# Optimization experiments

Measured on AMD Instinct MI355X. Metric: run time of the kernel, lower is better.

Reference implementation:

```python
import jax, jax.numpy as jnp
import numpy as np


def setup_inputs() -> dict:
    key = jax.random.key(0)
    k1, k2 = jax.random.split(key)
    B, H, S, D = 4, 16, 4096, 128
    tensor = jax.random.normal(k1, (B, H, S, D), dtype=jnp.float32)
    # per-head decay in (0, 1)
    gamma = jax.random.uniform(k2, (H,), dtype=jnp.float32)
    return {"tensor": tensor, "gamma": gamma}


def reference(tensor, gamma):
    """Discounted cumsum (left): y[b,h,t,d] = x[b,h,t,d] + gamma[h] * y[b,h,t-1,d].

    Implemented as a parallel associative scan over the sequence axis using the
    linear-recurrence monoid (a, b) o (a', b') = (a*a', a'*b + b').
    """
    # broadcast per-head gamma to element-wise decay coefficients  (B,H,S,D)
    a = jnp.broadcast_to(gamma[None, :, None, None], tensor.shape)

    def combine(c1, c2):
        a1, b1 = c1
        a2, b2 = c2
        return (a1 * a2, a2 * b1 + b2)

    _, y = jax.lax.associative_scan(combine, (a, tensor), axis=2)
    return y
```

## Files before the change

### kernel.cpp

```cpp
#include <hip/hip_runtime.h>

constexpr int B = 4, H = 16, S = 4096, D = 128;
constexpr int BH = B * H;
constexpr int CHUNKS = 128;
constexpr int L = S / CHUNKS;
constexpr int D4 = D / 4;
constexpr int UNITS = BH * CHUNKS;
constexpr int THREADS = UNITS * D4;
constexpr int NBLK = THREADS / 256;

typedef float f32x4 __attribute__((ext_vector_type(4)));

__device__ __forceinline__ float4 f4fma(float a, float4 x, float4 y) {
    float4 r;
    r.x = fmaf(a, x.x, y.x);
    r.y = fmaf(a, x.y, y.y);
    r.z = fmaf(a, x.z, y.z);
    r.w = fmaf(a, x.w, y.w);
    return r;
}

__device__ __forceinline__ void nt_store4(float4* p, float4 v) {
    union { float4 s; f32x4 v4; } u;
    u.s = v;
    __builtin_nontemporal_store(u.v4, (f32x4*)p);
}

__global__ __launch_bounds__(256) void dc_carry(const float4* __restrict__ x,
                                                const float* __restrict__ gamma,
                                                float4* __restrict__ carries) {
    const int tid  = blockIdx.x * 256 + threadIdx.x;
    const int l    = tid & (D4 - 1);
    const int unit = tid >> 5;
    const int bh   = unit >> 7;
    const float g  = gamma[bh & (H - 1)];

    const float lg = __logf(g);
    float kf = (-2.996f + __logf(1.0f - g)) / lg;
    int K = (int)ceilf(kf);
    K = max(1, min(L, K));

    const float4* pe = x + ((size_t)unit * L + (L - K)) * D4 + l;
    float4 carry = make_float4(0.f, 0.f, 0.f, 0.f);
    #pragma unroll 8
    for (int i = 0; i < K; ++i) {
        carry = f4fma(g, carry, pe[(size_t)i * D4]);
    }
    carries[(size_t)unit * D4 + l] = carry;
}

__global__ __launch_bounds__(256) void dc_scan(const float4* __restrict__ x,
                                               const float* __restrict__ gamma,
                                               const float4* __restrict__ carries,
                                               float4* __restrict__ y) {
    const int tid  = blockIdx.x * 256 + threadIdx.x;
    const int l    = tid & (D4 - 1);
    const int unit = tid >> 5;
    const int c    = unit & (CHUNKS - 1);
    const int bh   = unit >> 7;
    const float g  = gamma[bh & (H - 1)];

    float gL = g;
    #pragma unroll
    for (int k = 0; k < 5; ++k) gL *= gL;

    float wf = (-4.828f + __logf(1.0f - gL)) / __logf(gL);
    int W = min(c, max(1, (int)ceilf(wf)));

    const size_t base = (size_t)unit * (L * D4) + l;
    const float4* p = x + base;
    float4*       q = y + base;

    float4 v0 = p[0 * D4];
    float4 v1 = p[1 * D4];
    float4 v2 = p[2 * D4];
    float4 v3 = p[3 * D4];

    const float4* cp = carries + ((size_t)(bh * CHUNKS) + c - 1) * D4 + l;
    float4 P = make_float4(0.f, 0.f, 0.f, 0.f);
    float mult = 1.f;
    for (int k = 0; k < W; ++k) {
        P = f4fma(mult, cp[-(ptrdiff_t)k * D4], P);
        mult *= gL;
    }

    float4 run = P;
    run = f4fma(g, run, v0); nt_store4(q + 0 * D4, run);
    run = f4fma(g, run, v1); nt_store4(q + 1 * D4, run);
    run = f4fma(g, run, v2); nt_store4(q + 2 * D4, run);
    run = f4fma(g, run, v3); nt_store4(q + 3 * D4, run);
    #pragma unroll 7
    for (int i = 4; i < L; ++i) {
        run = f4fma(g, run, p[(size_t)i * D4]);
        nt_store4(q + (size_t)i * D4, run);
    }
}

extern "C" void kernel_launch(void* const* d_in, const int* in_sizes, int n_in,
                              void* d_out, int out_size, void* d_ws, size_t ws_size,
                              hipStream_t stream) {
    const float4* x     = (const float4*)d_in[0];
    const float*  gamma = (const float*)d_in[1];
    float4*       y     = (float4*)d_out;
    float4*       carries = (float4*)d_ws;

    dc_carry<<<NBLK, 256, 0, stream>>>(x, gamma, carries);
    dc_scan<<<NBLK, 256, 0, stream>>>(x, gamma, carries, y);
}
```

Baseline: 54.80 us.

## Fuse carry and scan kernels into one cooperative kernel with grid sync

Merges the carry-computation kernel and the scan kernel into a single kernel launched with hipLaunchCooperativeKernel. A grid-wide sync separates writing the per-chunk carries from reading them. This removes the second launch and the dependency gap between the two kernels. In exchange it requires all 1024 blocks to be co-resident and adds the cost of a grid barrier.

```diff
diff --git a/kernel.cpp b/kernel.cpp
--- a/kernel.cpp
+++ b/kernel.cpp
@@ -1,4 +1,7 @@
 #include <hip/hip_runtime.h>
+#include <hip/hip_cooperative_groups.h>
+
+namespace cg = cooperative_groups;
 
 constexpr int B = 4, H = 16, S = 4096, D = 128;
 constexpr int BH = B * H;
@@ -6,8 +9,7 @@
 constexpr int L = S / CHUNKS;
 constexpr int D4 = D / 4;
 constexpr int UNITS = BH * CHUNKS;
-constexpr int THREADS = UNITS * D4;
-constexpr int NBLK = THREADS / 256;
+constexpr int NBLK = UNITS * D4 / 256;
 
 typedef float f32x4 __attribute__((ext_vector_type(4)));
 
@@ -26,33 +28,10 @@
     __builtin_nontemporal_store(u.v4, (f32x4*)p);
 }
 
-__global__ __launch_bounds__(256) void dc_carry(const float4* __restrict__ x,
+__global__ __launch_bounds__(256) void dc_fused(const float4* __restrict__ x,
                                                 const float* __restrict__ gamma,
+                                                float4* __restrict__ y,
                                                 float4* __restrict__ carries) {
-    const int tid  = blockIdx.x * 256 + threadIdx.x;
-    const int l    = tid & (D4 - 1);
-    const int unit = tid >> 5;
-    const int bh   = unit >> 7;
-    const float g  = gamma[bh & (H - 1)];
-
-    const float lg = __logf(g);
-    float kf = (-2.996f + __logf(1.0f - g)) / lg;
-    int K = (int)ceilf(kf);
-    K = max(1, min(L, K));
-
-    const float4* pe = x + ((size_t)unit * L + (L - K)) * D4 + l;
-    float4 carry = make_float4(0.f, 0.f, 0.f, 0.f);
-    #pragma unroll 8
-    for (int i = 0; i < K; ++i) {
-        carry = f4fma(g, carry, pe[(size_t)i * D4]);
-    }
-    carries[(size_t)unit * D4 + l] = carry;
-}
-
-__global__ __launch_bounds__(256) void dc_scan(const float4* __restrict__ x,
-                                               const float* __restrict__ gamma,
-                                               const float4* __restrict__ carries,
-                                               float4* __restrict__ y) {
     const int tid  = blockIdx.x * 256 + threadIdx.x;
     const int l    = tid & (D4 - 1);
     const int unit = tid >> 5;
@@ -64,17 +43,30 @@
     #pragma unroll
     for (int k = 0; k < 5; ++k) gL *= gL;
 
-    float wf = (-4.828f + __logf(1.0f - gL)) / __logf(gL);
-    int W = min(c, max(1, (int)ceilf(wf)));
+    const float lg = __logf(g);
+    int K = (int)ceilf((-2.996f + __logf(1.0f - g)) / lg);
+    K = max(1, min(L, K));
 
     const size_t base = (size_t)unit * (L * D4) + l;
     const float4* p = x + base;
     float4*       q = y + base;
 
+    {
+        const float4* pe = p + (size_t)(L - K) * D4;
+        float4 A = make_float4(0.f, 0.f, 0.f, 0.f);
+        for (int i = 0; i < K; ++i) A = f4fma(g, A, pe[(size_t)i * D4]);
+        carries[(size_t)unit * D4 + l] = A;
+    }
+
+    cg::this_grid().sync();
+
     float4 v0 = p[0 * D4];
     float4 v1 = p[1 * D4];
     float4 v2 = p[2 * D4];
     float4 v3 = p[3 * D4];
+
+    float wf = (-4.828f + __logf(1.0f - gL)) / __logf(gL);
+    int W = min(c, max(1, (int)ceilf(wf)));
 
     const float4* cp = carries + ((size_t)(bh * CHUNKS) + c - 1) * D4 + l;
     float4 P = make_float4(0.f, 0.f, 0.f, 0.f);
@@ -104,6 +96,7 @@
     float4*       y     = (float4*)d_out;
     float4*       carries = (float4*)d_ws;
 
-    dc_carry<<<NBLK, 256, 0, stream>>>(x, gamma, carries);
-    dc_scan<<<NBLK, 256, 0, stream>>>(x, gamma, carries, y);
+    void* args[] = { (void*)&x, (void*)&gamma, (void*)&y, (void*)&carries };
+    hipLaunchCooperativeKernel((const void*)dc_fused, dim3(NBLK), dim3(256),
+                               args, 0, stream);
 }
```

New measurement: 166.8 us. 3.04x slower.
